# Kernel optimization log

Measured on AMD Instinct MI355X. Metric: run time of the kernel, lower is better.

The kernel has to match this reference:

```python
import jax, jax.numpy as jnp
import numpy as np

N, T, H, NENV, L = 8192, 48, 256, 10, 2
NIN = 1 + 2 + NENV + 1 + 2  # x, coords(2), env(NENV), areas, bird_uv(2) = 16


def setup_inputs() -> dict:
    key = jax.random.key(0)
    ks = jax.random.split(key, 10)
    x = jax.random.normal(ks[0], (N, T), dtype=jnp.float32)
    coords = jax.random.normal(ks[1], (N, 2), dtype=jnp.float32)
    env = jax.random.normal(ks[2], (N, NENV, T), dtype=jnp.float32)
    areas = jax.random.uniform(ks[3], (N,), dtype=jnp.float32)
    bird_uv = jax.random.normal(ks[4], (N, 2, T), dtype=jnp.float32)
    # input2hidden: Linear(NIN, H, bias=False), kaiming-normal (fan_in = NIN)
    W_in = jax.random.normal(ks[5], (H, NIN), dtype=jnp.float32) * np.sqrt(2.0 / NIN)
    # LSTMCell params per layer: weight_ih [4H,H], weight_hh [4H,H], biases [4H]
    k_lstm = 1.0 / np.sqrt(H)
    W_ih = jax.random.uniform(ks[6], (L, 4 * H, H), minval=-k_lstm, maxval=k_lstm, dtype=jnp.float32)
    W_hh = jax.random.uniform(ks[7], (L, 4 * H, H), minval=-k_lstm, maxval=k_lstm, dtype=jnp.float32)
    b_ih = jax.random.uniform(ks[8], (L, 4 * H), minval=-k_lstm, maxval=k_lstm, dtype=jnp.float32)
    b_hh = jax.random.uniform(ks[9], (L, 4 * H), minval=-k_lstm, maxval=k_lstm, dtype=jnp.float32)
    return {"x": x, "coords": coords, "env": env, "areas": areas, "bird_uv": bird_uv,
            "W_in": W_in, "W_ih": W_ih, "W_hh": W_hh, "b_ih": b_ih, "b_hh": b_hh}


def _lstm_cell(inp, h, c, w_ih, w_hh, bi, bh):
    # torch.nn.LSTMCell gate order: i, f, g, o
    gates = inp @ w_ih.T + bi + h @ w_hh.T + bh  # [N, 4H]
    i, f, g, o = jnp.split(gates, 4, axis=-1)
    i = jax.nn.sigmoid(i)
    f = jax.nn.sigmoid(f)
    g = jnp.tanh(g)
    o = jax.nn.sigmoid(o)
    c_new = f * c + i * g
    h_new = o * jnp.tanh(c_new)
    return h_new, c_new


def reference(x, coords, env, areas, bird_uv, W_in, W_ih, W_hh, b_ih, b_hh):
    # Build [N, NIN, T] feature tensor matching torch.cat([x, coords, env, areas, bird_uv], dim=1)
    feats = jnp.concatenate([
        x[:, None, :],                                            # [N,1,T]
        jnp.broadcast_to(coords[:, :, None], (N, 2, T)),          # [N,2,T]
        env,                                                      # [N,NENV,T]
        jnp.broadcast_to(areas[:, None, None], (N, 1, T)),        # [N,1,T]
        bird_uv,                                                  # [N,2,T]
    ], axis=1)
    # input2hidden applied to all timesteps at once: [T, N, H]
    proj = jnp.einsum('hf,nft->tnh', W_in, feats)

    def step(carry, inp_t):
        h, c = carry  # each [L, N, H]
        inp = inp_t
        hs, cs = [], []
        for l in range(L):  # dropout_p = 0 -> no dropout between layers
            hl, cl = _lstm_cell(inp, h[l], c[l], W_ih[l], W_hh[l], b_ih[l], b_hh[l])
            hs.append(hl)
            cs.append(cl)
            inp = hl
        return (jnp.stack(hs), jnp.stack(cs)), None

    h0 = jnp.zeros((L, N, H), dtype=x.dtype)
    c0 = jnp.zeros((L, N, H), dtype=x.dtype)
    (h, c), _ = jax.lax.scan(step, (h0, c0), proj)
    return h, c
```

## Files before the change

### kernel.cpp

```cpp
#include <hip/hip_runtime.h>
#include <hip/hip_bf16.h>
#include <cstdint>

#define NB 8192
#define TSTEPS 48

typedef __hip_bfloat16 bf16;
typedef short bf16x8 __attribute__((ext_vector_type(8)));
typedef float f32x4 __attribute__((ext_vector_type(4)));

__device__ __forceinline__ float sigf(float x) { return 1.0f / (1.0f + __expf(-x)); }
__device__ __forceinline__ float tanhf_fast(float x) { return 2.0f / (1.0f + __expf(-2.0f * x)) - 1.0f; }

__device__ __forceinline__ void gld_lds16(const void* g, void* l) {
  typedef const __attribute__((address_space(1))) unsigned int* gp_t;
  typedef __attribute__((address_space(3))) unsigned int* lp_t;
  __builtin_amdgcn_global_load_lds(reinterpret_cast<gp_t>(reinterpret_cast<uintptr_t>(g)),
                                   reinterpret_cast<lp_t>(reinterpret_cast<uintptr_t>(l)),
                                   16, 0, 0);
}

__global__ void feats_kernel(const float* __restrict__ x, const float* __restrict__ coords,
                             const float* __restrict__ env, const float* __restrict__ areas,
                             const float* __restrict__ bird, bf16* __restrict__ feats) {
  int idx = blockIdx.x * 256 + threadIdx.x;
  int n = idx & (NB - 1);
  int t = idx >> 13;
  __align__(16) bf16 v[32];
  v[0] = __float2bfloat16(x[n * TSTEPS + t]);
  v[1] = __float2bfloat16(coords[n * 2 + 0]);
  v[2] = __float2bfloat16(coords[n * 2 + 1]);
#pragma unroll
  for (int e = 0; e < 10; ++e) v[3 + e] = __float2bfloat16(env[(n * 10 + e) * TSTEPS + t]);
  v[13] = __float2bfloat16(areas[n]);
  v[14] = __float2bfloat16(bird[(n * 2 + 0) * TSTEPS + t]);
  v[15] = __float2bfloat16(bird[(n * 2 + 1) * TSTEPS + t]);
#pragma unroll
  for (int f = 16; f < 32; ++f) v[f] = __float2bfloat16(0.0f);
  bf16* dst = feats + (size_t)idx * 32;
#pragma unroll
  for (int c = 0; c < 4; ++c) ((bf16x8*)dst)[c] = ((const bf16x8*)v)[c];
}

__device__ __forceinline__ int orig_row(int jp) {
  int q = jp >> 7, g = (jp >> 5) & 3, s = jp & 31;
  return g * 256 + q * 32 + s;
}

__global__ void packA_kernel(const float* __restrict__ W_hh0, const float* __restrict__ W_ih0,
                             const float* __restrict__ W_in, bf16* __restrict__ WA) {
  int idx = blockIdx.x * 256 + threadIdx.x;
  int jp = idx / 288, col = idx % 288;
  int j = orig_row(jp);
  float val = 0.0f;
  if (col < 256) {
    val = W_hh0[j * 256 + col];
  } else if (col < 272) {
    int f = col - 256;
    float s = 0.0f;
    for (int k = 0; k < 256; ++k) s += W_ih0[j * 256 + k] * W_in[k * 16 + f];
    val = s;
  }
  WA[(size_t)jp * 288 + col] = __float2bfloat16(val);
}

__global__ void packB_kernel(const float* __restrict__ W_ih1, const float* __restrict__ W_hh1,
                             bf16* __restrict__ WB) {
  int idx = blockIdx.x * 256 + threadIdx.x;
  int jp = idx >> 9, col = idx & 511;
  int j = orig_row(jp);
  float val = (col < 256) ? W_ih1[j * 256 + col] : W_hh1[j * 256 + (col - 256)];
  WB[(size_t)jp * 512 + col] = __float2bfloat16(val);
}

__global__ void packBias_kernel(const float* __restrict__ b_ih, const float* __restrict__ b_hh,
                                float* __restrict__ bA, float* __restrict__ bB) {
  int idx = blockIdx.x * 256 + threadIdx.x;
  int layer = idx >> 10, jp = idx & 1023;
  int j = orig_row(jp);
  float v = b_ih[layer * 1024 + j] + b_hh[layer * 1024 + j];
  if (layer == 0) bA[jp] = v; else bB[jp] = v;
}

__global__ __launch_bounds__(256, 4) void lstm_step(
    const bf16* __restrict__ h0r, bf16* __restrict__ h0w,
    const bf16* __restrict__ h1r, bf16* __restrict__ h1w,
    const bf16* __restrict__ feats,
    const bf16* __restrict__ WA, const bf16* __restrict__ WB,
    const float* __restrict__ bA, const float* __restrict__ bB,
    bf16* __restrict__ c0, bf16* __restrict__ c1,
    float* __restrict__ out, int tA, int tB, int phase0, int lastA, int lastB) {
  __shared__ float Gs[64 * 132];
  bf16* As = (bf16*)Gs;
  bf16* Bs = As + 128 * 32;

  const int tid = threadIdx.x;
  const int wid = tid >> 6, lane = tid & 63;
  const int quad = lane >> 4, l16 = lane & 15;
  const int mb = (wid >> 1) * 64, nb = (wid & 1) * 64;
  const int rowbase = blockIdx.x * 128;
  const int q = blockIdx.y;
  const int isA = blockIdx.z + phase0;

  const bf16* Wp = isA ? WA : WB;
  const int KW = isA ? 288 : 512;
  const int KITERS = isA ? 9 : 16;
  const int t = isA ? tA : tB;

  f32x4 acc[4][4];
#pragma unroll
  for (int i = 0; i < 4; ++i)
#pragma unroll
    for (int j = 0; j < 4; ++j) acc[i][j] = f32x4{0.f, 0.f, 0.f, 0.f};

  const int arow = wid * 32 + (lane >> 2);
  const int achunk = (lane & 3) * 8;
  const bf16* WGrow = Wp + (size_t)(q * 128 + arow) * KW + achunk;
  bf16* lA = As + wid * 1024;
  bf16* lB = Bs + wid * 1024;

  for (int kb = 0; kb < KITERS; ++kb) {
    const bf16* Arow;
    int astr;
    if (isA && kb == 8) {
      Arow = feats + ((size_t)t * NB + rowbase) * 32;
      astr = 32;
    } else {
      const bf16* src = (!isA && kb >= 8) ? (h1r + (kb - 8) * 32) : (h0r + kb * 32);
      Arow = src + (size_t)rowbase * 256;
      astr = 256;
    }
    const bf16* ga = Arow + (size_t)arow * astr + achunk;
    const bf16* gb = WGrow + kb * 32;
    gld_lds16(ga, lA);
    gld_lds16(ga + (size_t)16 * astr, lA + 512);
    gld_lds16(gb, lB);
    gld_lds16(gb + (size_t)16 * KW, lB + 512);
    __syncthreads();
    bf16x8 af[4], bfr[4];
#pragma unroll
    for (int i = 0; i < 4; ++i) af[i] = *(const bf16x8*)&As[(mb + i * 16 + l16) * 32 + quad * 8];
#pragma unroll
    for (int j = 0; j < 4; ++j) bfr[j] = *(const bf16x8*)&Bs[(nb + j * 16 + l16) * 32 + quad * 8];
#pragma unroll
    for (int i = 0; i < 4; ++i)
#pragma unroll
      for (int j = 0; j < 4; ++j)
        acc[i][j] = __builtin_amdgcn_mfma_f32_16x16x32_bf16(af[i], bfr[j], acc[i][j], 0, 0, 0);
    __syncthreads();
  }

  const float* bias = isA ? bA : bB;
  bf16* cst = isA ? c0 : c1;
  bf16* hout = isA ? h0w : h1w;
  const int last = isA ? lastA : lastB;
  float* out_h = out + (size_t)(isA ? 0 : 1) * NB * 256;
  float* out_c = out + (size_t)(isA ? 2 : 3) * NB * 256;

  const int s = tid & 31;
  const int rg = tid >> 5;
  const float bi = bias[q * 128 + 0 + s];
  const float bf_ = bias[q * 128 + 32 + s];
  const float bg = bias[q * 128 + 64 + s];
  const float bo = bias[q * 128 + 96 + s];
  const int u = q * 32 + s;

  for (int half = 0; half < 2; ++half) {
    if ((wid >> 1) == half) {
#pragma unroll
      for (int i = 0; i < 4; ++i)
#pragma unroll
        for (int j = 0; j < 4; ++j)
#pragma unroll
          for (int r = 0; r < 4; ++r)
            Gs[(i * 16 + quad * 4 + r) * 132 + nb + j * 16 + l16] = acc[i][j][r];
    }
    __syncthreads();
#pragma unroll
    for (int it = 0; it < 8; ++it) {
      int rl = rg * 8 + it;
      int n = rowbase + half * 64 + rl;
      float gi = sigf(Gs[rl * 132 + 0 + s] + bi);
      float gf = sigf(Gs[rl * 132 + 32 + s] + bf_);
      float gg = tanhf_fast(Gs[rl * 132 + 64 + s] + bg);
      float go = sigf(Gs[rl * 132 + 96 + s] + bo);
      size_t ci = (size_t)n * 256 + u;
      float c = __bfloat162float(cst[ci]);
      float cn = gf * c + gi * gg;
      float hn = go * tanhf_fast(cn);
      if (!last) cst[ci] = __float2bfloat16(cn);
      hout[ci] = __float2bfloat16(hn);
      if (last) {
        out_h[ci] = hn;
        out_c[ci] = cn;
      }
    }
    __syncthreads();
  }
}

extern "C" void kernel_launch(void* const* d_in, const int* in_sizes, int n_in,
                              void* d_out, int out_size, void* d_ws, size_t ws_size,
                              hipStream_t stream) {
  const float* x = (const float*)d_in[0];
  const float* coords = (const float*)d_in[1];
  const float* env = (const float*)d_in[2];
  const float* areas = (const float*)d_in[3];
  const float* bird = (const float*)d_in[4];
  const float* W_in = (const float*)d_in[5];
  const float* W_ih = (const float*)d_in[6];
  const float* W_hh = (const float*)d_in[7];
  const float* b_ih = (const float*)d_in[8];
  const float* b_hh = (const float*)d_in[9];
  float* out = (float*)d_out;

  const size_t MB = 1 << 20;
  char* w0 = (char*)d_ws;
  auto H0 = [&](int i) { return (bf16*)(w0 + (size_t)i * 8 * MB); };
  auto H1 = [&](int i) { return (bf16*)(w0 + 4 * MB + (size_t)i * 8 * MB); };
  bf16* c0 = (bf16*)(w0 + 16 * MB);
  bf16* c1 = (bf16*)(w0 + 20 * MB);
  bf16* feats = (bf16*)(w0 + 24 * MB);
  bf16* WA = (bf16*)(w0 + 48 * MB);
  bf16* WB = (bf16*)(w0 + 49 * MB);
  float* bA = (float*)(w0 + 50 * MB);
  float* bB = (float*)(w0 + 50 * MB + 4096);

  hipMemsetAsync(w0 + 8 * MB, 0, 16 * MB, stream);

  feats_kernel<<<(NB * TSTEPS) / 256, 256, 0, stream>>>(x, coords, env, areas, bird, feats);
  packA_kernel<<<(1024 * 288) / 256, 256, 0, stream>>>(W_hh, W_ih, W_in, WA);
  packB_kernel<<<(1024 * 512) / 256, 256, 0, stream>>>(W_ih + 1024 * 256, W_hh + 1024 * 256, WB);
  packBias_kernel<<<2048 / 256, 256, 0, stream>>>(b_ih, b_hh, bA, bB);

  lstm_step<<<dim3(64, 8, 1), 256, 0, stream>>>(
      H0(1), H0(0), H1(0), H1(1), feats, WA, WB, bA, bB, c0, c1, out,
      0, 0, 1, 0, 0);
  for (int s2 = 0; s2 <= 46; ++s2) {
    int pa = (s2 + 1) & 1, pb = s2 & 1;
    lstm_step<<<dim3(64, 8, 2), 256, 0, stream>>>(
        H0(pb), H0(pa), H1(pa), H1(pb), feats, WA, WB, bA, bB, c0, c1, out,
        s2 + 1, s2, 0, (s2 == 46), 0);
  }
  lstm_step<<<dim3(64, 8, 1), 256, 0, stream>>>(
      H0(1), H0(0), H1(0), H1(1), feats, WA, WB, bA, bB, c0, c1, out,
      0, 47, 0, 0, 1);
}
```

Measured before the change: 1.441 ms.

## Fuse both LSTM layers per block with double-buffered LDS and in-register gates

Each block of the step kernel now computes both layer-0 and layer-1 gate GEMMs for the same 128-row by 256-gate tile: 512 threads, two accumulator sets, and K-tiles staged into double-buffered LDS so the next load overlaps the current MFMA work. Weight rows are reordered so each wave's accumulator columns already hold the i/f/g/o gates for the same hidden unit. This lets the cell update run directly from registers instead of going through an LDS round trip with extra barriers. LDS columns are XOR-swizzled in the packed weights, the feats buffer and the h writes to cut bank conflicts, and the grid block order is swizzled. The trade-off is higher register pressure from two accumulator sets and fewer, larger blocks.

After: 1.762 ms. 1.22x slower.

```diff
diff --git a/kernel.cpp b/kernel.cpp
--- a/kernel.cpp
+++ b/kernel.cpp
@@ -20,6 +20,15 @@
                                    16, 0, 0);
 }
 
+__device__ __forceinline__ int orig_row_p(int p) {
+  int ug = p >> 6, g = (p >> 4) & 3, s = p & 15;
+  return g * 256 + ug * 16 + s;
+}
+__device__ __forceinline__ int unswz_col(int colp, int r) {
+  int cc = ((colp >> 3) & 3) ^ ((r >> 1) & 3);
+  return (colp & ~31) | (cc << 3) | (colp & 7);
+}
+
 __global__ void feats_kernel(const float* __restrict__ x, const float* __restrict__ coords,
                              const float* __restrict__ env, const float* __restrict__ areas,
                              const float* __restrict__ bird, bf16* __restrict__ feats) {
@@ -38,165 +47,163 @@
 #pragma unroll
   for (int f = 16; f < 32; ++f) v[f] = __float2bfloat16(0.0f);
   bf16* dst = feats + (size_t)idx * 32;
-#pragma unroll
-  for (int c = 0; c < 4; ++c) ((bf16x8*)dst)[c] = ((const bf16x8*)v)[c];
-}
-
-__device__ __forceinline__ int orig_row(int jp) {
-  int q = jp >> 7, g = (jp >> 5) & 3, s = jp & 31;
-  return g * 256 + q * 32 + s;
+  int sw = (n >> 1) & 3;
+#pragma unroll
+  for (int c = 0; c < 4; ++c) ((bf16x8*)dst)[c ^ sw] = ((const bf16x8*)v)[c];
 }
 
 __global__ void packA_kernel(const float* __restrict__ W_hh0, const float* __restrict__ W_ih0,
                              const float* __restrict__ W_in, bf16* __restrict__ WA) {
   int idx = blockIdx.x * 256 + threadIdx.x;
-  int jp = idx / 288, col = idx % 288;
-  int j = orig_row(jp);
+  int p = idx / 288, colp = idx % 288;
+  int j = orig_row_p(p);
+  int k = unswz_col(colp, p);
   float val = 0.0f;
-  if (col < 256) {
-    val = W_hh0[j * 256 + col];
-  } else if (col < 272) {
-    int f = col - 256;
+  if (k < 256) {
+    val = W_hh0[j * 256 + k];
+  } else if (k < 272) {
+    int f = k - 256;
     float s = 0.0f;
-    for (int k = 0; k < 256; ++k) s += W_ih0[j * 256 + k] * W_in[k * 16 + f];
+    for (int kk = 0; kk < 256; ++kk) s += W_ih0[j * 256 + kk] * W_in[kk * 16 + f];
     val = s;
   }
-  WA[(size_t)jp * 288 + col] = __float2bfloat16(val);
+  WA[(size_t)p * 288 + colp] = __float2bfloat16(val);
 }
 
 __global__ void packB_kernel(const float* __restrict__ W_ih1, const float* __restrict__ W_hh1,
                              bf16* __restrict__ WB) {
   int idx = blockIdx.x * 256 + threadIdx.x;
-  int jp = idx >> 9, col = idx & 511;
-  int j = orig_row(jp);
-  float val = (col < 256) ? W_ih1[j * 256 + col] : W_hh1[j * 256 + (col - 256)];
-  WB[(size_t)jp * 512 + col] = __float2bfloat16(val);
+  int p = idx >> 9, colp = idx & 511;
+  int j = orig_row_p(p);
+  int k = unswz_col(colp, p);
+  float val = (k < 256) ? W_ih1[j * 256 + k] : W_hh1[j * 256 + (k - 256)];
+  WB[(size_t)p * 512 + colp] = __float2bfloat16(val);
 }
 
 __global__ void packBias_kernel(const float* __restrict__ b_ih, const float* __restrict__ b_hh,
                                 float* __restrict__ bA, float* __restrict__ bB) {
   int idx = blockIdx.x * 256 + threadIdx.x;
-  int layer = idx >> 10, jp = idx & 1023;
-  int j = orig_row(jp);
-  float v = b_ih[layer * 1024 + j] + b_hh[layer * 1024 + j];
-  if (layer == 0) bA[jp] = v; else bB[jp] = v;
-}
-
-__global__ __launch_bounds__(256, 4) void lstm_step(
+  int layer = idx >> 10, r = idx & 1023;
+  float v = b_ih[layer * 1024 + r] + b_hh[layer * 1024 + r];
+  if (layer == 0) bA[r] = v; else bB[r] = v;
+}
+
+__global__ __launch_bounds__(512, 2) void lstm_step(
     const bf16* __restrict__ h0r, bf16* __restrict__ h0w,
     const bf16* __restrict__ h1r, bf16* __restrict__ h1w,
     const bf16* __restrict__ feats,
     const bf16* __restrict__ WA, const bf16* __restrict__ WB,
     const float* __restrict__ bA, const float* __restrict__ bB,
     bf16* __restrict__ c0, bf16* __restrict__ c1,
-    float* __restrict__ out, int tA, int tB, int phase0, int lastA, int lastB) {
-  __shared__ float Gs[64 * 132];
-  bf16* As = (bf16*)Gs;
-  bf16* Bs = As + 128 * 32;
+    float* __restrict__ out, int tA, int tB, int doA, int doB, int lastA, int lastB) {
+  __shared__ __align__(16) bf16 As[2 * 128 * 32];
+  __shared__ __align__(16) bf16 Bs[2 * 256 * 32];
 
   const int tid = threadIdx.x;
   const int wid = tid >> 6, lane = tid & 63;
   const int quad = lane >> 4, l16 = lane & 15;
-  const int mb = (wid >> 1) * 64, nb = (wid & 1) * 64;
-  const int rowbase = blockIdx.x * 128;
-  const int q = blockIdx.y;
-  const int isA = blockIdx.z + phase0;
-
-  const bf16* Wp = isA ? WA : WB;
-  const int KW = isA ? 288 : 512;
-  const int KITERS = isA ? 9 : 16;
-  const int t = isA ? tA : tB;
-
-  f32x4 acc[4][4];
+  const int wr = wid >> 2, wc = wid & 3;
+
+  const int id = blockIdx.x;
+  const int swz = (id & 7) * 32 + (id >> 3);
+  const int rowbase = (swz >> 2) * 128;
+  const int q = swz & 3;
+
+  const int nB = doB ? 16 : 0;
+  const int NT = nB + (doA ? 9 : 0);
+
+  const int r4 = lane >> 2;
+  const int ch = (lane & 3) * 8;
+  const int cb = (quad ^ ((l16 >> 1) & 3)) * 8;
+
+  f32x4 accA[4][4], accB[4][4];
 #pragma unroll
   for (int i = 0; i < 4; ++i)
 #pragma unroll
-    for (int j = 0; j < 4; ++j) acc[i][j] = f32x4{0.f, 0.f, 0.f, 0.f};
-
-  const int arow = wid * 32 + (lane >> 2);
-  const int achunk = (lane & 3) * 8;
-  const bf16* WGrow = Wp + (size_t)(q * 128 + arow) * KW + achunk;
-  bf16* lA = As + wid * 1024;
-  bf16* lB = Bs + wid * 1024;
-
-  for (int kb = 0; kb < KITERS; ++kb) {
-    const bf16* Arow;
-    int astr;
-    if (isA && kb == 8) {
-      Arow = feats + ((size_t)t * NB + rowbase) * 32;
-      astr = 32;
+    for (int j = 0; j < 4; ++j) {
+      accA[i][j] = f32x4{0.f, 0.f, 0.f, 0.f};
+      accB[i][j] = f32x4{0.f, 0.f, 0.f, 0.f};
+    }
+
+  auto stage = [&](int it, int buf) {
+    const bf16* asrc; int astr;
+    if (it < nB) {
+      if (it < 8) { asrc = h0r + it * 32; astr = 256; }
+      else        { asrc = h1r + (it - 8) * 32; astr = 256; }
     } else {
-      const bf16* src = (!isA && kb >= 8) ? (h1r + (kb - 8) * 32) : (h0r + kb * 32);
-      Arow = src + (size_t)rowbase * 256;
-      astr = 256;
-    }
-    const bf16* ga = Arow + (size_t)arow * astr + achunk;
-    const bf16* gb = WGrow + kb * 32;
-    gld_lds16(ga, lA);
-    gld_lds16(ga + (size_t)16 * astr, lA + 512);
+      int ka = it - nB;
+      if (ka < 8) { asrc = h0r + ka * 32; astr = 256; }
+      else        { asrc = feats + (size_t)tA * (NB * 32); astr = 32; }
+    }
+    const bf16* ga = asrc + (size_t)(rowbase + wid * 16 + r4) * astr + ch;
+    gld_lds16(ga, As + buf * (128 * 32) + wid * (16 * 32));
+    const bf16* wsrc; int kw;
+    if (it < nB) { wsrc = WB + it * 32; kw = 512; }
+    else         { wsrc = WA + (it - nB) * 32; kw = 288; }
+    const bf16* gb = wsrc + (size_t)(q * 256 + wid * 32 + r4) * kw + ch;
+    bf16* lB = Bs + buf * (256 * 32) + wid * (32 * 32);
     gld_lds16(gb, lB);
-    gld_lds16(gb + (size_t)16 * KW, lB + 512);
-    __syncthreads();
+    gld_lds16(gb + (size_t)16 * kw, lB + 16 * 32);
+  };
+
+  stage(0, 0);
+  __syncthreads();
+
+  for (int it = 0; it < NT; ++it) {
+    const int buf = it & 1;
+    if (it + 1 < NT) stage(it + 1, buf ^ 1);
+    const bf16* Ab = As + buf * (128 * 32);
+    const bf16* Bb = Bs + buf * (256 * 32);
     bf16x8 af[4], bfr[4];
 #pragma unroll
-    for (int i = 0; i < 4; ++i) af[i] = *(const bf16x8*)&As[(mb + i * 16 + l16) * 32 + quad * 8];
-#pragma unroll
-    for (int j = 0; j < 4; ++j) bfr[j] = *(const bf16x8*)&Bs[(nb + j * 16 + l16) * 32 + quad * 8];
-#pragma unroll
     for (int i = 0; i < 4; ++i)
-#pragma unroll
-      for (int j = 0; j < 4; ++j)
-        acc[i][j] = __builtin_amdgcn_mfma_f32_16x16x32_bf16(af[i], bfr[j], acc[i][j], 0, 0, 0);
+      af[i] = *(const bf16x8*)(Ab + (wr * 64 + i * 16 + l16) * 32 + cb);
+#pragma unroll
+    for (int j = 0; j < 4; ++j)
+      bfr[j] = *(const bf16x8*)(Bb + (wc * 64 + j * 16 + l16) * 32 + cb);
+    if (it < nB) {
+#pragma unroll
+      for (int i = 0; i < 4; ++i)
+#pragma unroll
+        for (int j = 0; j < 4; ++j)
+          accB[i][j] = __builtin_amdgcn_mfma_f32_16x16x32_bf16(af[i], bfr[j], accB[i][j], 0, 0, 0);
+    } else {
+#pragma unroll
+      for (int i = 0; i < 4; ++i)
+#pragma unroll
+        for (int j = 0; j < 4; ++j)
+          accA[i][j] = __builtin_amdgcn_mfma_f32_16x16x32_bf16(af[i], bfr[j], accA[i][j], 0, 0, 0);
+    }
     __syncthreads();
   }
 
-  const float* bias = isA ? bA : bB;
-  bf16* cst = isA ? c0 : c1;
-  bf16* hout = isA ? h0w : h1w;
-  const int last = isA ? lastA : lastB;
-  float* out_h = out + (size_t)(isA ? 0 : 1) * NB * 256;
-  float* out_c = out + (size_t)(isA ? 2 : 3) * NB * 256;
-
-  const int s = tid & 31;
-  const int rg = tid >> 5;
-  const float bi = bias[q * 128 + 0 + s];
-  const float bf_ = bias[q * 128 + 32 + s];
-  const float bg = bias[q * 128 + 64 + s];
-  const float bo = bias[q * 128 + 96 + s];
-  const int u = q * 32 + s;
-
-  for (int half = 0; half < 2; ++half) {
-    if ((wid >> 1) == half) {
-#pragma unroll
-      for (int i = 0; i < 4; ++i)
-#pragma unroll
-        for (int j = 0; j < 4; ++j)
-#pragma unroll
-          for (int r = 0; r < 4; ++r)
-            Gs[(i * 16 + quad * 4 + r) * 132 + nb + j * 16 + l16] = acc[i][j][r];
-    }
-    __syncthreads();
-#pragma unroll
-    for (int it = 0; it < 8; ++it) {
-      int rl = rg * 8 + it;
-      int n = rowbase + half * 64 + rl;
-      float gi = sigf(Gs[rl * 132 + 0 + s] + bi);
-      float gf = sigf(Gs[rl * 132 + 32 + s] + bf_);
-      float gg = tanhf_fast(Gs[rl * 132 + 64 + s] + bg);
-      float go = sigf(Gs[rl * 132 + 96 + s] + bo);
-      size_t ci = (size_t)n * 256 + u;
-      float c = __bfloat162float(cst[ci]);
-      float cn = gf * c + gi * gg;
-      float hn = go * tanhf_fast(cn);
-      if (!last) cst[ci] = __float2bfloat16(cn);
-      hout[ci] = __float2bfloat16(hn);
-      if (last) {
-        out_h[ci] = hn;
-        out_c[ci] = cn;
+  const int u = (q * 4 + wc) * 16 + l16;
+  auto cell = [&](f32x4 (&acc)[4][4], const float* __restrict__ bias, bf16* __restrict__ cst,
+                  bf16* __restrict__ hout, int last, float* __restrict__ oh,
+                  float* __restrict__ oc) {
+    const float bi = bias[u], bf_ = bias[256 + u], bg = bias[512 + u], bo = bias[768 + u];
+#pragma unroll
+    for (int i = 0; i < 4; ++i) {
+#pragma unroll
+      for (int rr = 0; rr < 4; ++rr) {
+        const int n = rowbase + wr * 64 + i * 16 + quad * 4 + rr;
+        const size_t ci = (size_t)n * 256 + u;
+        float gi = sigf(acc[i][0][rr] + bi);
+        float gf = sigf(acc[i][1][rr] + bf_);
+        float gg = tanhf_fast(acc[i][2][rr] + bg);
+        float go = sigf(acc[i][3][rr] + bo);
+        float c = __bfloat162float(cst[ci]);
+        float cn = gf * c + gi * gg;
+        float hn = go * tanhf_fast(cn);
+        if (!last) cst[ci] = __float2bfloat16(cn);
+        const int col = (u & ~31) | (((((u >> 3) & 3) ^ ((n >> 1) & 3))) << 3) | (u & 7);
+        hout[(size_t)n * 256 + col] = __float2bfloat16(hn);
+        if (last) { oh[ci] = hn; oc[ci] = cn; }
       }
     }
-    __syncthreads();
-  }
+  };
+  if (doB) cell(accB, bB, c1, h1w, lastB, out + (size_t)NB * 256, out + (size_t)3 * NB * 256);
+  if (doA) cell(accA, bA, c0, h0w, lastA, out, out + (size_t)2 * NB * 256);
 }
 
 extern "C" void kernel_launch(void* const* d_in, const int* in_sizes, int n_in,
@@ -233,16 +240,12 @@
   packB_kernel<<<(1024 * 512) / 256, 256, 0, stream>>>(W_ih + 1024 * 256, W_hh + 1024 * 256, WB);
   packBias_kernel<<<2048 / 256, 256, 0, stream>>>(b_ih, b_hh, bA, bB);
 
-  lstm_step<<<dim3(64, 8, 1), 256, 0, stream>>>(
-      H0(1), H0(0), H1(0), H1(1), feats, WA, WB, bA, bB, c0, c1, out,
-      0, 0, 1, 0, 0);
-  for (int s2 = 0; s2 <= 46; ++s2) {
-    int pa = (s2 + 1) & 1, pb = s2 & 1;
-    lstm_step<<<dim3(64, 8, 2), 256, 0, stream>>>(
-        H0(pb), H0(pa), H1(pa), H1(pb), feats, WA, WB, bA, bB, c0, c1, out,
-        s2 + 1, s2, 0, (s2 == 46), 0);
+  for (int s = 0; s <= 48; ++s) {
+    lstm_step<<<dim3(256), 512, 0, stream>>>(
+        H0((s + 1) & 1), H0(s & 1), H1(s & 1), H1((s + 1) & 1),
+        feats, WA, WB, bA, bB, c0, c1, out,
+        s, s - 1,
+        (s <= 47) ? 1 : 0, (s >= 1) ? 1 : 0,
+        (s == 47) ? 1 : 0, (s == 48) ? 1 : 0);
   }
-  lstm_step<<<dim3(64, 8, 1), 256, 0, stream>>>(
-      H0(1), H0(0), H1(0), H1(1), feats, WA, WB, bA, bB, c0, c1, out,
-      0, 47, 0, 0, 1);
-}
+}
```
